# Kernel tuning notes

Hardware: AMD Instinct MI355X
Metric: run time of the kernel (lower is better)

## Reference

```python
import math
import jax, jax.numpy as jnp
import numpy as np

B, T, D_MODEL, HEAD_DIM = 4, 2048, 768, 64

def setup_inputs() -> dict:
    key = jax.random.key(0)
    ks = jax.random.split(key, 4)
    scale = 1.0 / math.sqrt(D_MODEL)
    return {
        "x": jax.random.normal(ks[0], (B, T, D_MODEL), dtype=jnp.float32),
        "Wq": jax.random.normal(ks[1], (D_MODEL, HEAD_DIM), dtype=jnp.float32) * scale,
        "bq": jnp.zeros((HEAD_DIM,), dtype=jnp.float32),
        "Wk": jax.random.normal(ks[2], (D_MODEL, HEAD_DIM), dtype=jnp.float32) * scale,
        "bk": jnp.zeros((HEAD_DIM,), dtype=jnp.float32),
        "Wv": jax.random.normal(ks[3], (D_MODEL, HEAD_DIM), dtype=jnp.float32) * scale,
        "bv": jnp.zeros((HEAD_DIM,), dtype=jnp.float32),
    }

def reference(x, Wq, bq, Wk, bk, Wv, bv):
    # Single causal self-attention head (dropout=0 / eval mode).
    q = x @ Wq + bq                      # [B, T, H]
    k = x @ Wk + bk                      # [B, T, H]
    v = x @ Wv + bv                      # [B, T, H]
    head_dim = q.shape[-1]
    scores = jnp.einsum("bth,bsh->bts", q, k) / math.sqrt(head_dim)  # [B, T, T]
    seq_len = x.shape[1]
    causal = jnp.tril(jnp.ones((seq_len, seq_len), dtype=bool))      # [T, T]
    scores = jnp.where(causal, scores, -jnp.inf)
    attn = jax.nn.softmax(scores, axis=-1)                           # [B, T, T]
    out = jnp.einsum("bts,bsh->bth", attn, v)                        # [B, T, H]
    return out
```

## Files before the change

kernel.cpp:

```cpp
#include <hip/hip_runtime.h>
#include <math.h>

#define BB 4
#define TT 2048
#define DM 768
#define HD 64
#define NROW (BB*TT)
#define WFRAG_HALF ((size_t)12*24*512)

typedef __attribute__((ext_vector_type(8))) short bf16x8;
typedef __attribute__((ext_vector_type(4))) float f32x4;

__device__ __forceinline__ unsigned short f2bf(float f) {
    unsigned int u = __float_as_uint(f);
    u += 0x7FFFu + ((u >> 16) & 1u);
    return (unsigned short)(u >> 16);
}
__device__ __forceinline__ float bf2f(unsigned short h) {
    return __uint_as_float(((unsigned int)h) << 16);
}

__global__ __launch_bounds__(256) void wconv_kernel(
    const float* __restrict__ Wq, const float* __restrict__ Wk,
    const float* __restrict__ Wv, unsigned short* __restrict__ wfrag)
{
    __shared__ float ws[32][69];
    const int blk = blockIdx.x;
    const int m = blk / 24, kc = blk % 24;
    const float* Wm = (m == 0) ? Wq : ((m == 1) ? Wk : Wv);
    const float sc = (m == 0) ? 0.125f : 1.0f;
    const int tid = threadIdx.x;
    {
        int r = tid >> 3, c0 = (tid & 7) * 8;
        *(float4*)&ws[r][c0]     = *(const float4*)(Wm + (size_t)(32*kc + r)*HD + c0);
        *(float4*)&ws[r][c0 + 4] = *(const float4*)(Wm + (size_t)(32*kc + r)*HD + c0 + 4);
    }
    __syncthreads();
    const int ntm = tid >> 6, lane = tid & 63;
    const int q15 = lane & 15, g = lane >> 4;
    const int col = 16*ntm + q15;
    bf16x8 hi, lo;
    #pragma unroll
    for (int j = 0; j < 8; ++j) {
        float w = ws[8*g + j][col] * sc;
        unsigned short h = f2bf(w);
        hi[j] = (short)h;
        lo[j] = (short)f2bf(w - bf2f(h));
    }
    size_t base = ((size_t)((m*4 + ntm)*24 + kc))*512 + (size_t)lane*8;
    *(bf16x8*)(wfrag + base) = hi;
    *(bf16x8*)(wfrag + WFRAG_HALF + base) = lo;
}

__global__ __launch_bounds__(512) void proj_mfma_kernel(
    const float* __restrict__ x, const unsigned short* __restrict__ wfrag,
    const float* __restrict__ bq, const float* __restrict__ bk,
    const float* __restrict__ bv,
    unsigned short* __restrict__ qo, unsigned short* __restrict__ ko,
    unsigned short* __restrict__ vT)
{
    __shared__ unsigned short xsh[2][2][32][132];
    const int tid  = threadIdx.x;
    const int wv   = tid >> 6;
    const int lane = tid & 63;
    const int q15  = lane & 15;
    const int g    = lane >> 4;
    const int row0 = blockIdx.x * 32;
    const int mt   = wv & 1;
    const int nt0  = 3 * (wv >> 1);
    const int xrow = 16*mt + q15;

    const int srow = tid >> 4;
    const int sc0  = (tid & 15) * 8;
    const float* xrp = x + (size_t)(row0 + srow)*DM + sc0;

    f32x4 acc[3];
    #pragma unroll
    for (int i = 0; i < 3; ++i) acc[i] = (f32x4){0.f, 0.f, 0.f, 0.f};

    {
        float4 xa = *(const float4*)(xrp);
        float4 xb = *(const float4*)(xrp + 4);
        bf16x8 hi, lo;
        float f[8] = {xa.x, xa.y, xa.z, xa.w, xb.x, xb.y, xb.z, xb.w};
        #pragma unroll
        for (int e = 0; e < 8; ++e) {
            unsigned short h = f2bf(f[e]);
            hi[e] = (short)h;
            lo[e] = (short)f2bf(f[e] - bf2f(h));
        }
        *(bf16x8*)&xsh[0][0][srow][sc0] = hi;
        *(bf16x8*)&xsh[0][1][srow][sc0] = lo;
    }
    __syncthreads();

    for (int t = 0; t < 6; ++t) {
        const int buf = t & 1;
        float4 xa, xb;
        if (t < 5) {
            xa = *(const float4*)(xrp + (t+1)*128);
            xb = *(const float4*)(xrp + (t+1)*128 + 4);
        }
        #pragma unroll
        for (int sub = 0; sub < 4; ++sub) {
            const int kcg = t*4 + sub;
            bf16x8 xfh = *(const bf16x8*)&xsh[buf][0][xrow][32*sub + 8*g];
            bf16x8 xfl = *(const bf16x8*)&xsh[buf][1][xrow][32*sub + 8*g];
            #pragma unroll
            for (int i = 0; i < 3; ++i) {
                const unsigned short* wp = wfrag + ((size_t)((nt0 + i)*24 + kcg))*512 + (size_t)lane*8;
                bf16x8 wh = *(const bf16x8*)wp;
                bf16x8 wl = *(const bf16x8*)(wp + WFRAG_HALF);
                acc[i] = __builtin_amdgcn_mfma_f32_16x16x32_bf16(xfh, wh, acc[i], 0, 0, 0);
                acc[i] = __builtin_amdgcn_mfma_f32_16x16x32_bf16(xfl, wh, acc[i], 0, 0, 0);
                acc[i] = __builtin_amdgcn_mfma_f32_16x16x32_bf16(xfh, wl, acc[i], 0, 0, 0);
            }
        }
        if (t < 5) {
            bf16x8 hi, lo;
            float f[8] = {xa.x, xa.y, xa.z, xa.w, xb.x, xb.y, xb.z, xb.w};
            #pragma unroll
            for (int e = 0; e < 8; ++e) {
                unsigned short h = f2bf(f[e]);
                hi[e] = (short)h;
                lo[e] = (short)f2bf(f[e] - bf2f(h));
            }
            *(bf16x8*)&xsh[buf^1][0][srow][sc0] = hi;
            *(bf16x8*)&xsh[buf^1][1][srow][sc0] = lo;
            __syncthreads();
        }
    }

    const int b  = row0 >> 11;
    const int t0 = row0 & 2047;
    #pragma unroll
    for (int i = 0; i < 3; ++i) {
        int nt = nt0 + i, m = nt >> 2, ntm = nt & 3;
        int col = 16*ntm + q15;
        float bb = (m == 0) ? 0.125f*bq[col] : ((m == 1) ? bk[col] : bv[col]);
        if (m == 2) {
            ushort4 pk;
            pk.x = f2bf(acc[i][0] + bb);
            pk.y = f2bf(acc[i][1] + bb);
            pk.z = f2bf(acc[i][2] + bb);
            pk.w = f2bf(acc[i][3] + bb);
            *(ushort4*)(vT + ((size_t)b*HD + col)*TT + t0 + 16*mt + 4*g) = pk;
        } else {
            unsigned short* op = (m == 0) ? qo : ko;
            #pragma unroll
            for (int r = 0; r < 4; ++r)
                op[(size_t)(row0 + 16*mt + 4*g + r)*HD + col] = f2bf(acc[i][r] + bb);
        }
    }
}

__global__ __launch_bounds__(256) void attn_mfma_kernel(
    const unsigned short* __restrict__ qb_, const unsigned short* __restrict__ kb_,
    const unsigned short* __restrict__ vt_, float* __restrict__ out)
{
    __shared__ unsigned short plds[4][16][40];
    __shared__ float olds[4][16][66];
    __shared__ float mlds[4][16][2];

    const int tid  = threadIdx.x;
    const int wv   = tid >> 6;
    const int lane = tid & 63;
    const int q15  = lane & 15;
    const int g    = lane >> 4;

    const int bx = blockIdx.x;
    const int b  = bx & 3;
    const int qt = (TT/16 - 1) - (bx >> 2);
    const int qbase = qt * 16;
    const int nk = qbase + 16;

    const unsigned short* qp = qb_ + (size_t)b*TT*HD;
    const unsigned short* kp = kb_ + (size_t)b*TT*HD;
    const unsigned short* vp = vt_ + (size_t)b*HD*TT;

    bf16x8 qf[2];
    #pragma unroll
    for (int c = 0; c < 2; ++c)
        qf[c] = *(const bf16x8*)(qp + (size_t)(qbase + q15)*HD + 32*c + 8*g);

    f32x4 accv[4];
    #pragma unroll
    for (int h = 0; h < 4; ++h) accv[h] = (f32x4){0.f, 0.f, 0.f, 0.f};
    float m = -INFINITY, l = 0.f;

    const int ck = ((nk + 127) >> 7) << 5;
    const int kstart = wv * ck;
    const int kend = min(kstart + ck, nk);

    for (int k0 = kstart; k0 < kend; k0 += 32) {
        bf16x8 vf[4];
        #pragma unroll
        for (int h = 0; h < 4; ++h)
            vf[h] = *(const bf16x8*)(vp + (size_t)(16*h + q15)*TT + k0 + 8*g);
        bf16x8 kf[2][2];
        #pragma unroll
        for (int t = 0; t < 2; ++t)
            #pragma unroll
            for (int c = 0; c < 2; ++c)
                kf[t][c] = *(const bf16x8*)(kp + (size_t)(k0 + 16*t + q15)*HD + 32*c + 8*g);

        f32x4 st[2];
        #pragma unroll
        for (int t = 0; t < 2; ++t) {
            f32x4 z = {0.f, 0.f, 0.f, 0.f};
            st[t] = __builtin_amdgcn_mfma_f32_16x16x32_bf16(kf[t][0], qf[0], z, 0, 0, 0);
            st[t] = __builtin_amdgcn_mfma_f32_16x16x32_bf16(kf[t][1], qf[1], st[t], 0, 0, 0);
        }
        if (k0 + 31 > qbase) {
            int qabs = qbase + q15;
            #pragma unroll
            for (int t = 0; t < 2; ++t)
                #pragma unroll
                for (int r = 0; r < 4; ++r)
                    if (k0 + 16*t + 4*g + r > qabs) st[t][r] = -INFINITY;
        }
        float pmax = st[0][0];
        #pragma unroll
        for (int t = 0; t < 2; ++t)
            #pragma unroll
            for (int r = 0; r < 4; ++r) pmax = fmaxf(pmax, st[t][r]);
        pmax = fmaxf(pmax, __shfl_xor(pmax, 16));
        pmax = fmaxf(pmax, __shfl_xor(pmax, 32));
        float mnew = fmaxf(m, pmax);
        float mc = fmaxf(mnew, -1e30f);
        float alpha = __expf(m - mc);
        float p[2][4];
        float psum = 0.f;
        #pragma unroll
        for (int t = 0; t < 2; ++t)
            #pragma unroll
            for (int r = 0; r < 4; ++r) {
                p[t][r] = __expf(st[t][r] - mc);
                psum += p[t][r];
            }
        psum += __shfl_xor(psum, 16);
        psum += __shfl_xor(psum, 32);
        l = l * alpha + psum;
        m = mnew;
        float av[4];
        #pragma unroll
        for (int r = 0; r < 4; ++r) av[r] = __shfl(alpha, 4*g + r);
        #pragma unroll
        for (int h = 0; h < 4; ++h)
            #pragma unroll
            for (int r = 0; r < 4; ++r) accv[h][r] *= av[r];
        #pragma unroll
        for (int t = 0; t < 2; ++t) {
            ushort4 pk;
            pk.x = f2bf(p[t][0]); pk.y = f2bf(p[t][1]);
            pk.z = f2bf(p[t][2]); pk.w = f2bf(p[t][3]);
            *(ushort4*)&plds[wv][q15][16*t + 4*g] = pk;
        }
        bf16x8 pa = *(const bf16x8*)&plds[wv][q15][8*g];
        #pragma unroll
        for (int h = 0; h < 4; ++h)
            accv[h] = __builtin_amdgcn_mfma_f32_16x16x32_bf16(pa, vf[h], accv[h], 0, 0, 0);
    }

    #pragma unroll
    for (int h = 0; h < 4; ++h)
        #pragma unroll
        for (int r = 0; r < 4; ++r)
            olds[wv][4*g + r][16*h + q15] = accv[h][r];
    if (g == 0) { mlds[wv][q15][0] = m; mlds[wv][q15][1] = l; }
    __syncthreads();

    {
        int qq = tid >> 4;
        int c4 = (tid & 15) << 2;
        float mw[4], lw[4];
        #pragma unroll
        for (int w = 0; w < 4; ++w) { mw[w] = mlds[w][qq][0]; lw[w] = mlds[w][qq][1]; }
        float M = fmaxf(fmaxf(mw[0], mw[1]), fmaxf(mw[2], mw[3]));
        float Mc = fmaxf(M, -1e30f);
        float ww[4], ltot = 0.f;
        #pragma unroll
        for (int w = 0; w < 4; ++w) { ww[w] = __expf(mw[w] - Mc); ltot += ww[w]*lw[w]; }
        float invl = 1.f / ltot;
        float4 o;
        #pragma unroll
        for (int e = 0; e < 4; ++e) {
            float s = 0.f;
            #pragma unroll
            for (int w = 0; w < 4; ++w) s += ww[w] * olds[w][qq][c4 + e];
            ((float*)&o)[e] = s * invl;
        }
        *(float4*)(out + ((size_t)b*TT + qbase + qq)*HD + c4) = o;
    }
}

extern "C" void kernel_launch(void* const* d_in, const int* in_sizes, int n_in,
                              void* d_out, int out_size, void* d_ws, size_t ws_size,
                              hipStream_t stream) {
    const float* x  = (const float*)d_in[0];
    const float* Wq = (const float*)d_in[1];
    const float* bq = (const float*)d_in[2];
    const float* Wk = (const float*)d_in[3];
    const float* bk = (const float*)d_in[4];
    const float* Wv = (const float*)d_in[5];
    const float* bv = (const float*)d_in[6];
    float* out = (float*)d_out;

    unsigned short* qbf   = (unsigned short*)d_ws;
    unsigned short* kbf   = qbf + (size_t)NROW*HD;
    unsigned short* vT    = kbf + (size_t)NROW*HD;
    unsigned short* wfrag = vT  + (size_t)NROW*HD;

    wconv_kernel<<<72, 256, 0, stream>>>(Wq, Wk, Wv, wfrag);
    proj_mfma_kernel<<<NROW/32, 512, 0, stream>>>(x, wfrag, bq, bk, bv, qbf, kbf, vT);
    attn_mfma_kernel<<<dim3(TT/16 * BB), 256, 0, stream>>>(qbf, kbf, vT, out);
}
```

Measured before the change: 50.95 us.

## Stage weight fragments through LDS with async global_load_lds double buffering

The projection kernel now converts the whole 32x768 x tile to hi/lo bf16 in shared memory up front. Weight fragments are reordered k-chunk-major and streamed into a double-buffered LDS region with global_load_lds, so each block fetches every weight fragment once instead of each wave reading it from global memory. This adds a barrier per k-chunk (24 instead of 6) and uses more shared memory, which may lower occupancy.

```diff
diff --git a/kernel.cpp b/kernel.cpp
--- a/kernel.cpp
+++ b/kernel.cpp
@@ -6,7 +6,7 @@
 #define DM 768
 #define HD 64
 #define NROW (BB*TT)
-#define WFRAG_HALF ((size_t)12*24*512)
+#define WFRAG_HALF ((size_t)24*12*512)
 
 typedef __attribute__((ext_vector_type(8))) short bf16x8;
 typedef __attribute__((ext_vector_type(4))) float f32x4;
@@ -18,6 +18,12 @@
 }
 __device__ __forceinline__ float bf2f(unsigned short h) {
     return __uint_as_float(((unsigned int)h) << 16);
+}
+
+__device__ __forceinline__ void g2lds16(const unsigned short* g, unsigned short* l) {
+    __builtin_amdgcn_global_load_lds(
+        (const __attribute__((address_space(1))) unsigned int*)g,
+        (__attribute__((address_space(3))) unsigned int*)l, 16, 0, 0);
 }
 
 __global__ __launch_bounds__(256) void wconv_kernel(
@@ -47,7 +53,7 @@
         hi[j] = (short)h;
         lo[j] = (short)f2bf(w - bf2f(h));
     }
-    size_t base = ((size_t)((m*4 + ntm)*24 + kc))*512 + (size_t)lane*8;
+    size_t base = ((size_t)(kc*12 + m*4 + ntm))*512 + (size_t)lane*8;
     *(bf16x8*)(wfrag + base) = hi;
     *(bf16x8*)(wfrag + WFRAG_HALF + base) = lo;
 }
@@ -59,7 +65,8 @@
     unsigned short* __restrict__ qo, unsigned short* __restrict__ ko,
     unsigned short* __restrict__ vT)
 {
-    __shared__ unsigned short xsh[2][2][32][132];
+    __shared__ unsigned short xsh[2][32][776];
+    __shared__ unsigned short wsh[2][24*512];
     const int tid  = threadIdx.x;
     const int wv   = tid >> 6;
     const int lane = tid & 63;
@@ -70,65 +77,64 @@
     const int nt0  = 3 * (wv >> 1);
     const int xrow = 16*mt + q15;
 
-    const int srow = tid >> 4;
-    const int sc0  = (tid & 15) * 8;
-    const float* xrp = x + (size_t)(row0 + srow)*DM + sc0;
+    {
+        const int r  = tid >> 4;
+        const int c4 = (tid & 15) * 4;
+        const float* xp = x + (size_t)(row0 + r)*DM + c4;
+        #pragma unroll
+        for (int p = 0; p < 12; ++p) {
+            float4 xv = *(const float4*)(xp + 64*p);
+            float f[4] = {xv.x, xv.y, xv.z, xv.w};
+            ushort4 hi, lo;
+            unsigned short h;
+            h = f2bf(f[0]); hi.x = h; lo.x = f2bf(f[0] - bf2f(h));
+            h = f2bf(f[1]); hi.y = h; lo.y = f2bf(f[1] - bf2f(h));
+            h = f2bf(f[2]); hi.z = h; lo.z = f2bf(f[2] - bf2f(h));
+            h = f2bf(f[3]); hi.w = h; lo.w = f2bf(f[3] - bf2f(h));
+            *(ushort4*)&xsh[0][r][c4 + 64*p] = hi;
+            *(ushort4*)&xsh[1][r][c4 + 64*p] = lo;
+        }
+    }
+    #pragma unroll
+    for (int jj = 0; jj < 3; ++jj) {
+        int j = 3*wv + jj;
+        const unsigned short* src = wfrag
+            + (j < 12 ? (size_t)j*512 : WFRAG_HALF + (size_t)(j - 12)*512)
+            + (size_t)lane*8;
+        g2lds16(src, &wsh[0][j*512]);
+    }
+    __syncthreads();
 
     f32x4 acc[3];
     #pragma unroll
     for (int i = 0; i < 3; ++i) acc[i] = (f32x4){0.f, 0.f, 0.f, 0.f};
 
-    {
-        float4 xa = *(const float4*)(xrp);
-        float4 xb = *(const float4*)(xrp + 4);
-        bf16x8 hi, lo;
-        float f[8] = {xa.x, xa.y, xa.z, xa.w, xb.x, xb.y, xb.z, xb.w};
-        #pragma unroll
-        for (int e = 0; e < 8; ++e) {
-            unsigned short h = f2bf(f[e]);
-            hi[e] = (short)h;
-            lo[e] = (short)f2bf(f[e] - bf2f(h));
-        }
-        *(bf16x8*)&xsh[0][0][srow][sc0] = hi;
-        *(bf16x8*)&xsh[0][1][srow][sc0] = lo;
-    }
-    __syncthreads();
-
-    for (int t = 0; t < 6; ++t) {
-        const int buf = t & 1;
-        float4 xa, xb;
-        if (t < 5) {
-            xa = *(const float4*)(xrp + (t+1)*128);
-            xb = *(const float4*)(xrp + (t+1)*128 + 4);
-        }
-        #pragma unroll
-        for (int sub = 0; sub < 4; ++sub) {
-            const int kcg = t*4 + sub;
-            bf16x8 xfh = *(const bf16x8*)&xsh[buf][0][xrow][32*sub + 8*g];
-            bf16x8 xfl = *(const bf16x8*)&xsh[buf][1][xrow][32*sub + 8*g];
-            #pragma unroll
-            for (int i = 0; i < 3; ++i) {
-                const unsigned short* wp = wfrag + ((size_t)((nt0 + i)*24 + kcg))*512 + (size_t)lane*8;
-                bf16x8 wh = *(const bf16x8*)wp;
-                bf16x8 wl = *(const bf16x8*)(wp + WFRAG_HALF);
-                acc[i] = __builtin_amdgcn_mfma_f32_16x16x32_bf16(xfh, wh, acc[i], 0, 0, 0);
-                acc[i] = __builtin_amdgcn_mfma_f32_16x16x32_bf16(xfl, wh, acc[i], 0, 0, 0);
-                acc[i] = __builtin_amdgcn_mfma_f32_16x16x32_bf16(xfh, wl, acc[i], 0, 0, 0);
+    for (int kcg = 0; kcg < 24; ++kcg) {
+        const int buf = kcg & 1;
+        if (kcg < 23) {
+            const int kn = kcg + 1;
+            #pragma unroll
+            for (int jj = 0; jj < 3; ++jj) {
+                int j = 3*wv + jj;
+                const unsigned short* src = wfrag
+                    + (j < 12 ? (size_t)(kn*12 + j)*512
+                              : WFRAG_HALF + (size_t)(kn*12 + j - 12)*512)
+                    + (size_t)lane*8;
+                g2lds16(src, &wsh[buf^1][j*512]);
             }
         }
-        if (t < 5) {
-            bf16x8 hi, lo;
-            float f[8] = {xa.x, xa.y, xa.z, xa.w, xb.x, xb.y, xb.z, xb.w};
-            #pragma unroll
-            for (int e = 0; e < 8; ++e) {
-                unsigned short h = f2bf(f[e]);
-                hi[e] = (short)h;
-                lo[e] = (short)f2bf(f[e] - bf2f(h));
-            }
-            *(bf16x8*)&xsh[buf^1][0][srow][sc0] = hi;
-            *(bf16x8*)&xsh[buf^1][1][srow][sc0] = lo;
-            __syncthreads();
-        }
+        bf16x8 xfh = *(const bf16x8*)&xsh[0][xrow][kcg*32 + 8*g];
+        bf16x8 xfl = *(const bf16x8*)&xsh[1][xrow][kcg*32 + 8*g];
+        #pragma unroll
+        for (int i = 0; i < 3; ++i) {
+            const int nt = nt0 + i;
+            bf16x8 wh = *(const bf16x8*)&wsh[buf][nt*512 + lane*8];
+            bf16x8 wl = *(const bf16x8*)&wsh[buf][(12 + nt)*512 + lane*8];
+            acc[i] = __builtin_amdgcn_mfma_f32_16x16x32_bf16(xfh, wh, acc[i], 0, 0, 0);
+            acc[i] = __builtin_amdgcn_mfma_f32_16x16x32_bf16(xfl, wh, acc[i], 0, 0, 0);
+            acc[i] = __builtin_amdgcn_mfma_f32_16x16x32_bf16(xfh, wl, acc[i], 0, 0, 0);
+        }
+        __syncthreads();
     }
 
     const int b  = row0 >> 11;
```

Measured after the change: 55.40 us. +8.7%, slower.

## Split projection blocks across Q/K/V and drop LDS staging of x

Applied to the files above, without the earlier changes.

The projection kernel now launches three 256-thread blocks per 32-row tile, one each for Q, K and V, instead of one 512-thread block covering all outputs. Each wave reads x straight from global memory into MFMA fragments, dropping the double-buffered shared staging and its barriers. The weight fragment layout is reordered so kc is the outer index. x is split into bf16 hi/lo by truncation rather than round-to-nearest. Outputs go through a small shared buffer so global stores are coalesced. The cost is that x is read three times from global memory, and truncation may change rounding slightly.

```diff
diff --git a/kernel.cpp b/kernel.cpp
--- a/kernel.cpp
+++ b/kernel.cpp
@@ -6,7 +6,7 @@
 #define DM 768
 #define HD 64
 #define NROW (BB*TT)
-#define WFRAG_HALF ((size_t)12*24*512)
+#define WFRAG_HALF ((size_t)24*12*512)
 
 typedef __attribute__((ext_vector_type(8))) short bf16x8;
 typedef __attribute__((ext_vector_type(4))) float f32x4;
@@ -47,110 +47,100 @@
         hi[j] = (short)h;
         lo[j] = (short)f2bf(w - bf2f(h));
     }
-    size_t base = ((size_t)((m*4 + ntm)*24 + kc))*512 + (size_t)lane*8;
+    size_t base = ((size_t)(kc*12 + m*4 + ntm))*512 + (size_t)lane*8;
     *(bf16x8*)(wfrag + base) = hi;
     *(bf16x8*)(wfrag + WFRAG_HALF + base) = lo;
 }
 
-__global__ __launch_bounds__(512) void proj_mfma_kernel(
+__global__ __launch_bounds__(256, 3) void proj_mfma_kernel(
     const float* __restrict__ x, const unsigned short* __restrict__ wfrag,
     const float* __restrict__ bq, const float* __restrict__ bk,
     const float* __restrict__ bv,
     unsigned short* __restrict__ qo, unsigned short* __restrict__ ko,
     unsigned short* __restrict__ vT)
 {
-    __shared__ unsigned short xsh[2][2][32][132];
+    __shared__ unsigned short stg[2304];
     const int tid  = threadIdx.x;
     const int wv   = tid >> 6;
     const int lane = tid & 63;
     const int q15  = lane & 15;
     const int g    = lane >> 4;
-    const int row0 = blockIdx.x * 32;
+    const int bx   = blockIdx.x;
+    const int nb   = bx % 3;
+    const int row0 = (bx / 3) * 32;
     const int mt   = wv & 1;
-    const int nt0  = 3 * (wv >> 1);
-    const int xrow = 16*mt + q15;
-
-    const int srow = tid >> 4;
-    const int sc0  = (tid & 15) * 8;
-    const float* xrp = x + (size_t)(row0 + srow)*DM + sc0;
-
-    f32x4 acc[3];
-    #pragma unroll
-    for (int i = 0; i < 3; ++i) acc[i] = (f32x4){0.f, 0.f, 0.f, 0.f};
-
-    {
-        float4 xa = *(const float4*)(xrp);
-        float4 xb = *(const float4*)(xrp + 4);
-        bf16x8 hi, lo;
+    const int np   = wv >> 1;
+    const int ntg0 = nb*4 + 2*np;
+
+    const float* xp = x + (size_t)(row0 + 16*mt + q15)*DM + 8*g;
+
+    f32x4 acc[2];
+    acc[0] = (f32x4){0.f, 0.f, 0.f, 0.f};
+    acc[1] = (f32x4){0.f, 0.f, 0.f, 0.f};
+
+    for (int kcg = 0; kcg < 24; ++kcg) {
+        float4 xa = *(const float4*)(xp + 32*kcg);
+        float4 xb = *(const float4*)(xp + 32*kcg + 4);
+        bf16x8 xfh, xfl;
         float f[8] = {xa.x, xa.y, xa.z, xa.w, xb.x, xb.y, xb.z, xb.w};
         #pragma unroll
         for (int e = 0; e < 8; ++e) {
-            unsigned short h = f2bf(f[e]);
-            hi[e] = (short)h;
-            lo[e] = (short)f2bf(f[e] - bf2f(h));
-        }
-        *(bf16x8*)&xsh[0][0][srow][sc0] = hi;
-        *(bf16x8*)&xsh[0][1][srow][sc0] = lo;
-    }
-    __syncthreads();
-
-    for (int t = 0; t < 6; ++t) {
-        const int buf = t & 1;
-        float4 xa, xb;
-        if (t < 5) {
-            xa = *(const float4*)(xrp + (t+1)*128);
-            xb = *(const float4*)(xrp + (t+1)*128 + 4);
-        }
-        #pragma unroll
-        for (int sub = 0; sub < 4; ++sub) {
-            const int kcg = t*4 + sub;
-            bf16x8 xfh = *(const bf16x8*)&xsh[buf][0][xrow][32*sub + 8*g];
-            bf16x8 xfl = *(const bf16x8*)&xsh[buf][1][xrow][32*sub + 8*g];
-            #pragma unroll
-            for (int i = 0; i < 3; ++i) {
-                const unsigned short* wp = wfrag + ((size_t)((nt0 + i)*24 + kcg))*512 + (size_t)lane*8;
-                bf16x8 wh = *(const bf16x8*)wp;
-                bf16x8 wl = *(const bf16x8*)(wp + WFRAG_HALF);
-                acc[i] = __builtin_amdgcn_mfma_f32_16x16x32_bf16(xfh, wh, acc[i], 0, 0, 0);
-                acc[i] = __builtin_amdgcn_mfma_f32_16x16x32_bf16(xfl, wh, acc[i], 0, 0, 0);
-                acc[i] = __builtin_amdgcn_mfma_f32_16x16x32_bf16(xfh, wl, acc[i], 0, 0, 0);
-            }
-        }
-        if (t < 5) {
-            bf16x8 hi, lo;
-            float f[8] = {xa.x, xa.y, xa.z, xa.w, xb.x, xb.y, xb.z, xb.w};
-            #pragma unroll
-            for (int e = 0; e < 8; ++e) {
-                unsigned short h = f2bf(f[e]);
-                hi[e] = (short)h;
-                lo[e] = (short)f2bf(f[e] - bf2f(h));
-            }
-            *(bf16x8*)&xsh[buf^1][0][srow][sc0] = hi;
-            *(bf16x8*)&xsh[buf^1][1][srow][sc0] = lo;
-            __syncthreads();
-        }
-    }
-
-    const int b  = row0 >> 11;
-    const int t0 = row0 & 2047;
-    #pragma unroll
-    for (int i = 0; i < 3; ++i) {
-        int nt = nt0 + i, m = nt >> 2, ntm = nt & 3;
-        int col = 16*ntm + q15;
-        float bb = (m == 0) ? 0.125f*bq[col] : ((m == 1) ? bk[col] : bv[col]);
-        if (m == 2) {
-            ushort4 pk;
-            pk.x = f2bf(acc[i][0] + bb);
-            pk.y = f2bf(acc[i][1] + bb);
-            pk.z = f2bf(acc[i][2] + bb);
-            pk.w = f2bf(acc[i][3] + bb);
-            *(ushort4*)(vT + ((size_t)b*HD + col)*TT + t0 + 16*mt + 4*g) = pk;
-        } else {
-            unsigned short* op = (m == 0) ? qo : ko;
+            unsigned short h = (unsigned short)(__float_as_uint(f[e]) >> 16);
+            float r = f[e] - bf2f(h);
+            xfh[e] = (short)h;
+            xfl[e] = (short)(unsigned short)(__float_as_uint(r) >> 16);
+        }
+        #pragma unroll
+        for (int i = 0; i < 2; ++i) {
+            const unsigned short* wp = wfrag + ((size_t)(kcg*12 + ntg0 + i))*512 + (size_t)lane*8;
+            bf16x8 wh = *(const bf16x8*)wp;
+            bf16x8 wl = *(const bf16x8*)(wp + WFRAG_HALF);
+            acc[i] = __builtin_amdgcn_mfma_f32_16x16x32_bf16(xfh, wh, acc[i], 0, 0, 0);
+            acc[i] = __builtin_amdgcn_mfma_f32_16x16x32_bf16(xfl, wh, acc[i], 0, 0, 0);
+            acc[i] = __builtin_amdgcn_mfma_f32_16x16x32_bf16(xfh, wl, acc[i], 0, 0, 0);
+        }
+    }
+
+    if (nb < 2) {
+        const float* bp = (nb == 0) ? bq : bk;
+        const float bsc = (nb == 0) ? 0.125f : 1.0f;
+        #pragma unroll
+        for (int i = 0; i < 2; ++i) {
+            int col = 16*(2*np + i) + q15;
+            float bb = bsc * bp[col];
             #pragma unroll
             for (int r = 0; r < 4; ++r)
-                op[(size_t)(row0 + 16*mt + 4*g + r)*HD + col] = f2bf(acc[i][r] + bb);
-        }
+                stg[(size_t)(16*mt + 4*g + r)*68 + col] = f2bf(acc[i][r] + bb);
+        }
+        __syncthreads();
+        const int rr = tid >> 3;
+        const int c8 = (tid & 7) * 8;
+        ushort4 a  = *(const ushort4*)&stg[(size_t)rr*68 + c8];
+        ushort4 b2 = *(const ushort4*)&stg[(size_t)rr*68 + c8 + 4];
+        unsigned short* op = (nb == 0) ? qo : ko;
+        *(ushort4*)(op + (size_t)(row0 + rr)*HD + c8)     = a;
+        *(ushort4*)(op + (size_t)(row0 + rr)*HD + c8 + 4) = b2;
+    } else {
+        #pragma unroll
+        for (int i = 0; i < 2; ++i) {
+            int h = 16*(2*np + i) + q15;
+            float bb = bv[h];
+            ushort4 v4;
+            v4.x = f2bf(acc[i][0] + bb);
+            v4.y = f2bf(acc[i][1] + bb);
+            v4.z = f2bf(acc[i][2] + bb);
+            v4.w = f2bf(acc[i][3] + bb);
+            *(ushort4*)&stg[(size_t)h*36 + 16*mt + 4*g] = v4;
+        }
+        __syncthreads();
+        const int h  = tid >> 2;
+        const int tg = (tid & 3) * 8;
+        const int b  = row0 >> 11;
+        const int t0 = row0 & 2047;
+        ushort4 a  = *(const ushort4*)&stg[(size_t)h*36 + tg];
+        ushort4 b2 = *(const ushort4*)&stg[(size_t)h*36 + tg + 4];
+        *(ushort4*)(vT + ((size_t)b*HD + h)*TT + t0 + tg)     = a;
+        *(ushort4*)(vT + ((size_t)b*HD + h)*TT + t0 + tg + 4) = b2;
     }
 }
 
@@ -312,6 +302,6 @@
     unsigned short* wfrag = vT  + (size_t)NROW*HD;
 
     wconv_kernel<<<72, 256, 0, stream>>>(Wq, Wk, Wv, wfrag);
-    proj_mfma_kernel<<<NROW/32, 512, 0, stream>>>(x, wfrag, bq, bk, bv, qbf, kbf, vT);
+    proj_mfma_kernel<<<768, 256, 0, stream>>>(x, wfrag, bq, bk, bv, qbf, kbf, vT);
     attn_mfma_kernel<<<dim3(TT/16 * BB), 256, 0, stream>>>(qbf, kbf, vT, out);
 }
```

Result: slower. 61.22 us (+20.2%).
